# Performance work log

Hardware: AMD Instinct MI355X
Metric: run time of the kernel (lower is better)

## Reference

```python
import jax, jax.numpy as jnp
import numpy as np

B, T, J, D = 32, 1024, 256, 512

def setup_inputs() -> dict:
    key = jax.random.key(0)
    k1, k2, k3 = jax.random.split(key, 3)
    h = jax.random.normal(k1, (B, T, D), dtype=jnp.float32)
    u = jax.random.normal(k2, (B, J, D), dtype=jnp.float32)
    w = jax.random.normal(k3, (1, 3 * D), dtype=jnp.float32) * 0.05
    return {"h": h, "u": u, "w": w}

def reference(h, u, w):
    # S[b,i,j] = w . concat([h_i, u_j, h_i*u_j])
    # Algebraic decomposition: w = [w_h, w_u, w_m]
    d = h.shape[-1]
    w = w[0]
    w_h, w_u, w_m = w[:d], w[d:2*d], w[2*d:]
    # [B,T,1] + [B,1,J] + [B,T,J]
    term_h = jnp.einsum('btd,d->bt', h, w_h)[:, :, None]
    term_u = jnp.einsum('bjd,d->bj', u, w_u)[:, None, :]
    term_m = jnp.einsum('btd,bjd->btj', h * w_m, u)
    return term_h + term_u + term_m
```

## Files before the change

### kernel.cpp

```cpp
#include <hip/hip_runtime.h>
#include <hip/hip_bf16.h>
#include <stdint.h>

#define B_ 32
#define T_ 1024
#define J_ 256
#define D_ 512

typedef __attribute__((ext_vector_type(8))) short short8;
typedef __attribute__((ext_vector_type(4))) float floatx4;

__global__ __launch_bounds__(256) void prep_kernel(
    const float* __restrict__ h, const float* __restrict__ u,
    const float* __restrict__ w,
    __hip_bfloat16* __restrict__ A, __hip_bfloat16* __restrict__ Bu,
    float* __restrict__ th, float* __restrict__ tu)
{
    int row  = blockIdx.x * 4 + (threadIdx.x >> 6);
    int lane = threadIdx.x & 63;
    const float* src;
    const float* wsum;
    const float* wmul;
    __hip_bfloat16* dst;
    float* tdst;
    if (row < B_ * T_) {
        src  = h + (size_t)row * D_;
        wsum = w;
        wmul = w + 2 * D_;
        dst  = A + (size_t)row * D_;
        tdst = th + row;
    } else {
        int r = row - B_ * T_;
        src  = u + (size_t)r * D_;
        wsum = w + D_;
        wmul = nullptr;
        dst  = Bu + (size_t)r * D_;
        tdst = tu + r;
    }
    int base = lane * 8;
    float4 v0  = *(const float4*)(src  + base);
    float4 v1  = *(const float4*)(src  + base + 4);
    float4 ws0 = *(const float4*)(wsum + base);
    float4 ws1 = *(const float4*)(wsum + base + 4);
    float s = v0.x*ws0.x + v0.y*ws0.y + v0.z*ws0.z + v0.w*ws0.w
            + v1.x*ws1.x + v1.y*ws1.y + v1.z*ws1.z + v1.w*ws1.w;

    float vals[8] = {v0.x, v0.y, v0.z, v0.w, v1.x, v1.y, v1.z, v1.w};
    if (wmul) {
        float4 m0 = *(const float4*)(wmul + base);
        float4 m1 = *(const float4*)(wmul + base + 4);
        vals[0]*=m0.x; vals[1]*=m0.y; vals[2]*=m0.z; vals[3]*=m0.w;
        vals[4]*=m1.x; vals[5]*=m1.y; vals[6]*=m1.z; vals[7]*=m1.w;
    }
    union { __hip_bfloat16 b[8]; uint4 q; } pk;
#pragma unroll
    for (int i = 0; i < 8; i++) pk.b[i] = __float2bfloat16(vals[i]);
    *(uint4*)(dst + base) = pk.q;

#pragma unroll
    for (int off = 32; off > 0; off >>= 1) s += __shfl_down(s, off, 64);
    if (lane == 0) *tdst = s;
}

__device__ inline void gload_lds16(const void* g, void* l) {
    __builtin_amdgcn_global_load_lds(
        (__attribute__((address_space(1))) void*)(g),
        (__attribute__((address_space(3))) void*)(l),
        16, 0, 0);
}

__global__ __launch_bounds__(256) void gemm_kernel(
    const __hip_bfloat16* __restrict__ A,
    const __hip_bfloat16* __restrict__ Bu,
    const float* __restrict__ th,
    const float* __restrict__ tu,
    float* __restrict__ out)
{
    __shared__ __align__(16) __hip_bfloat16 sA[128 * 32];
    __shared__ __align__(16) __hip_bfloat16 sB[128 * 32];

    const int b   = blockIdx.y;
    const int tM  = blockIdx.x >> 1;
    const int tN  = blockIdx.x & 1;
    const int tid = threadIdx.x;
    const int w = tid >> 6, lane = tid & 63;
    const int wr = w >> 1, wc = w & 1;

    const __hip_bfloat16* Ab = A  + ((size_t)b * T_ + tM * 128) * D_;
    const __hip_bfloat16* Bb = Bu + ((size_t)b * J_ + tN * 128) * D_;

    const int sr = tid >> 2;
    const int sc = (tid & 3) * 8;
    const int ldsOff = tid * 8;

    floatx4 acc[4][4];
#pragma unroll
    for (int i = 0; i < 4; i++)
#pragma unroll
        for (int j = 0; j < 4; j++) acc[i][j] = (floatx4)0.0f;

    const int kb = (lane >> 4) * 8;
    const int fr = lane & 15;

    for (int k0 = 0; k0 < D_; k0 += 32) {
        gload_lds16(Ab + (size_t)sr        * D_ + k0 + sc, sA + ldsOff);
        gload_lds16(Ab + (size_t)(sr + 64) * D_ + k0 + sc, sA + 64 * 32 + ldsOff);
        gload_lds16(Bb + (size_t)sr        * D_ + k0 + sc, sB + ldsOff);
        gload_lds16(Bb + (size_t)(sr + 64) * D_ + k0 + sc, sB + 64 * 32 + ldsOff);
        __syncthreads();

        short8 af[4], bfr[4];
#pragma unroll
        for (int mi = 0; mi < 4; mi++)
            af[mi] = *(const short8*)(sA + (wr * 64 + mi * 16 + fr) * 32 + kb);
#pragma unroll
        for (int ni = 0; ni < 4; ni++)
            bfr[ni] = *(const short8*)(sB + (wc * 64 + ni * 16 + fr) * 32 + kb);
#pragma unroll
        for (int mi = 0; mi < 4; mi++)
#pragma unroll
            for (int ni = 0; ni < 4; ni++)
                acc[mi][ni] = __builtin_amdgcn_mfma_f32_16x16x32_bf16(
                    af[mi], bfr[ni], acc[mi][ni], 0, 0, 0);
        __syncthreads();
    }

    const size_t outB = (size_t)b * T_ * J_;
    const int colq = lane & 15;
    const int rq   = (lane >> 4) * 4;
    const float* thb = th + b * T_;
    const float* tub = tu + b * J_;
#pragma unroll
    for (int mi = 0; mi < 4; mi++) {
        int r0 = tM * 128 + wr * 64 + mi * 16 + rq;
#pragma unroll
        for (int ni = 0; ni < 4; ni++) {
            int col = tN * 128 + wc * 64 + ni * 16 + colq;
            float tuv = tub[col];
#pragma unroll
            for (int r = 0; r < 4; r++) {
                out[outB + (size_t)(r0 + r) * J_ + col] =
                    acc[mi][ni][r] + thb[r0 + r] + tuv;
            }
        }
    }
}

extern "C" void kernel_launch(void* const* d_in, const int* in_sizes, int n_in,
                              void* d_out, int out_size, void* d_ws, size_t ws_size,
                              hipStream_t stream)
{
    const float* h = (const float*)d_in[0];
    const float* u = (const float*)d_in[1];
    const float* w = (const float*)d_in[2];
    float* out = (float*)d_out;

    uint8_t* ws = (uint8_t*)d_ws;
    __hip_bfloat16* A  = (__hip_bfloat16*)ws;
    __hip_bfloat16* Bu = (__hip_bfloat16*)(ws + (size_t)B_*T_*D_*2);
    float* th = (float*)(ws + (size_t)B_*T_*D_*2 + (size_t)B_*J_*D_*2);
    float* tu = th + B_*T_;

    prep_kernel<<<dim3((B_*T_ + B_*J_) / 4), 256, 0, stream>>>(h, u, w, A, Bu, th, tu);

    gemm_kernel<<<dim3((T_/128)*(J_/128), B_), 256, 0, stream>>>(A, Bu, th, tu, out);
}
```

Baseline: 140.0 us.

## Fold w_h and w_m into u operand and read h directly in GEMM

Rewrites the score as h·(u*w_m + w_h) + u·w_u, so the h row term becomes part of the GEMM and only u needs preprocessing. The GEMM now loads fp32 h from global memory, converts it to bf16 in registers and stores it to LDS. This removes the large h-to-bf16 prep pass and its workspace round trip. The cost is that h tiles are reread in fp32 for each of the two N tiles, using synchronous loads without the async LDS path, and the h·w_h term now also goes through bf16 rounding.

```diff
diff --git a/kernel.cpp b/kernel.cpp
--- a/kernel.cpp
+++ b/kernel.cpp
@@ -10,56 +10,41 @@
 typedef __attribute__((ext_vector_type(8))) short short8;
 typedef __attribute__((ext_vector_type(4))) float floatx4;
 
-__global__ __launch_bounds__(256) void prep_kernel(
-    const float* __restrict__ h, const float* __restrict__ u,
-    const float* __restrict__ w,
-    __hip_bfloat16* __restrict__ A, __hip_bfloat16* __restrict__ Bu,
-    float* __restrict__ th, float* __restrict__ tu)
+__global__ __launch_bounds__(256) void prep_u_kernel(
+    const float* __restrict__ u, const float* __restrict__ w,
+    __hip_bfloat16* __restrict__ B2, float* __restrict__ tu)
 {
     int row  = blockIdx.x * 4 + (threadIdx.x >> 6);
     int lane = threadIdx.x & 63;
-    const float* src;
-    const float* wsum;
-    const float* wmul;
-    __hip_bfloat16* dst;
-    float* tdst;
-    if (row < B_ * T_) {
-        src  = h + (size_t)row * D_;
-        wsum = w;
-        wmul = w + 2 * D_;
-        dst  = A + (size_t)row * D_;
-        tdst = th + row;
-    } else {
-        int r = row - B_ * T_;
-        src  = u + (size_t)r * D_;
-        wsum = w + D_;
-        wmul = nullptr;
-        dst  = Bu + (size_t)r * D_;
-        tdst = tu + r;
-    }
+    const float* src = u + (size_t)row * D_;
     int base = lane * 8;
-    float4 v0  = *(const float4*)(src  + base);
-    float4 v1  = *(const float4*)(src  + base + 4);
-    float4 ws0 = *(const float4*)(wsum + base);
-    float4 ws1 = *(const float4*)(wsum + base + 4);
-    float s = v0.x*ws0.x + v0.y*ws0.y + v0.z*ws0.z + v0.w*ws0.w
-            + v1.x*ws1.x + v1.y*ws1.y + v1.z*ws1.z + v1.w*ws1.w;
 
-    float vals[8] = {v0.x, v0.y, v0.z, v0.w, v1.x, v1.y, v1.z, v1.w};
-    if (wmul) {
-        float4 m0 = *(const float4*)(wmul + base);
-        float4 m1 = *(const float4*)(wmul + base + 4);
-        vals[0]*=m0.x; vals[1]*=m0.y; vals[2]*=m0.z; vals[3]*=m0.w;
-        vals[4]*=m1.x; vals[5]*=m1.y; vals[6]*=m1.z; vals[7]*=m1.w;
-    }
+    float4 v0  = *(const float4*)(src + base);
+    float4 v1  = *(const float4*)(src + base + 4);
+    float4 wh0 = *(const float4*)(w + base);
+    float4 wh1 = *(const float4*)(w + base + 4);
+    float4 wu0 = *(const float4*)(w + D_ + base);
+    float4 wu1 = *(const float4*)(w + D_ + base + 4);
+    float4 wm0 = *(const float4*)(w + 2*D_ + base);
+    float4 wm1 = *(const float4*)(w + 2*D_ + base + 4);
+
+    float s = v0.x*wu0.x + v0.y*wu0.y + v0.z*wu0.z + v0.w*wu0.w
+            + v1.x*wu1.x + v1.y*wu1.y + v1.z*wu1.z + v1.w*wu1.w;
+
+    float vals[8] = {
+        v0.x*wm0.x + wh0.x, v0.y*wm0.y + wh0.y,
+        v0.z*wm0.z + wh0.z, v0.w*wm0.w + wh0.w,
+        v1.x*wm1.x + wh1.x, v1.y*wm1.y + wh1.y,
+        v1.z*wm1.z + wh1.z, v1.w*wm1.w + wh1.w };
+
     union { __hip_bfloat16 b[8]; uint4 q; } pk;
 #pragma unroll
     for (int i = 0; i < 8; i++) pk.b[i] = __float2bfloat16(vals[i]);
-    *(uint4*)(dst + base) = pk.q;
+    *(uint4*)(B2 + (size_t)row * D_ + base) = pk.q;
 
 #pragma unroll
     for (int off = 32; off > 0; off >>= 1) s += __shfl_down(s, off, 64);
-    if (lane == 0) *tdst = s;
+    if (lane == 0) tu[row] = s;
 }
 
 __device__ inline void gload_lds16(const void* g, void* l) {
@@ -70,9 +55,8 @@
 }
 
 __global__ __launch_bounds__(256) void gemm_kernel(
-    const __hip_bfloat16* __restrict__ A,
-    const __hip_bfloat16* __restrict__ Bu,
-    const float* __restrict__ th,
+    const float* __restrict__ h,
+    const __hip_bfloat16* __restrict__ B2,
     const float* __restrict__ tu,
     float* __restrict__ out)
 {
@@ -86,12 +70,15 @@
     const int w = tid >> 6, lane = tid & 63;
     const int wr = w >> 1, wc = w & 1;
 
-    const __hip_bfloat16* Ab = A  + ((size_t)b * T_ + tM * 128) * D_;
-    const __hip_bfloat16* Bb = Bu + ((size_t)b * J_ + tN * 128) * D_;
+    const float*          Ah = h  + ((size_t)b * T_ + tM * 128) * D_;
+    const __hip_bfloat16* Bb = B2 + ((size_t)b * J_ + tN * 128) * D_;
 
     const int sr = tid >> 2;
     const int sc = (tid & 3) * 8;
-    const int ldsOff = tid * 8;
+    const int ldsOffB = tid * 8;
+
+    const int ar = tid >> 1;
+    const int ac = (tid & 1) * 16;
 
     floatx4 acc[4][4];
 #pragma unroll
@@ -103,10 +90,28 @@
     const int fr = lane & 15;
 
     for (int k0 = 0; k0 < D_; k0 += 32) {
-        gload_lds16(Ab + (size_t)sr        * D_ + k0 + sc, sA + ldsOff);
-        gload_lds16(Ab + (size_t)(sr + 64) * D_ + k0 + sc, sA + 64 * 32 + ldsOff);
-        gload_lds16(Bb + (size_t)sr        * D_ + k0 + sc, sB + ldsOff);
-        gload_lds16(Bb + (size_t)(sr + 64) * D_ + k0 + sc, sB + 64 * 32 + ldsOff);
+        gload_lds16(Bb + (size_t)sr        * D_ + k0 + sc, sB + ldsOffB);
+        gload_lds16(Bb + (size_t)(sr + 64) * D_ + k0 + sc, sB + 64 * 32 + ldsOffB);
+
+        {
+            const float* ap = Ah + (size_t)ar * D_ + k0 + ac;
+            float4 a0 = *(const float4*)(ap);
+            float4 a1 = *(const float4*)(ap + 4);
+            float4 a2 = *(const float4*)(ap + 8);
+            float4 a3 = *(const float4*)(ap + 12);
+            union { __hip_bfloat16 b[16]; uint4 q[2]; } pk;
+            pk.b[0]=__float2bfloat16(a0.x); pk.b[1]=__float2bfloat16(a0.y);
+            pk.b[2]=__float2bfloat16(a0.z); pk.b[3]=__float2bfloat16(a0.w);
+            pk.b[4]=__float2bfloat16(a1.x); pk.b[5]=__float2bfloat16(a1.y);
+            pk.b[6]=__float2bfloat16(a1.z); pk.b[7]=__float2bfloat16(a1.w);
+            pk.b[8]=__float2bfloat16(a2.x); pk.b[9]=__float2bfloat16(a2.y);
+            pk.b[10]=__float2bfloat16(a2.z); pk.b[11]=__float2bfloat16(a2.w);
+            pk.b[12]=__float2bfloat16(a3.x); pk.b[13]=__float2bfloat16(a3.y);
+            pk.b[14]=__float2bfloat16(a3.z); pk.b[15]=__float2bfloat16(a3.w);
+            uint4* dst = (uint4*)(sA + ar * 32 + ac);
+            dst[0] = pk.q[0];
+            dst[1] = pk.q[1];
+        }
         __syncthreads();
 
         short8 af[4], bfr[4];
@@ -128,7 +133,6 @@
     const size_t outB = (size_t)b * T_ * J_;
     const int colq = lane & 15;
     const int rq   = (lane >> 4) * 4;
-    const float* thb = th + b * T_;
     const float* tub = tu + b * J_;
 #pragma unroll
     for (int mi = 0; mi < 4; mi++) {
@@ -140,7 +144,7 @@
 #pragma unroll
             for (int r = 0; r < 4; r++) {
                 out[outB + (size_t)(r0 + r) * J_ + col] =
-                    acc[mi][ni][r] + thb[r0 + r] + tuv;
+                    acc[mi][ni][r] + tuv;
             }
         }
     }
@@ -156,12 +160,10 @@
     float* out = (float*)d_out;
 
     uint8_t* ws = (uint8_t*)d_ws;
-    __hip_bfloat16* A  = (__hip_bfloat16*)ws;
-    __hip_bfloat16* Bu = (__hip_bfloat16*)(ws + (size_t)B_*T_*D_*2);
-    float* th = (float*)(ws + (size_t)B_*T_*D_*2 + (size_t)B_*J_*D_*2);
-    float* tu = th + B_*T_;
+    __hip_bfloat16* B2 = (__hip_bfloat16*)ws;
+    float* tu = (float*)(ws + (size_t)B_ * J_ * D_ * 2);
 
-    prep_kernel<<<dim3((B_*T_ + B_*J_) / 4), 256, 0, stream>>>(h, u, w, A, Bu, th, tu);
+    prep_u_kernel<<<dim3(B_ * J_ / 4), 256, 0, stream>>>(u, w, B2, tu);
 
-    gemm_kernel<<<dim3((T_/128)*(J_/128), B_), 256, 0, stream>>>(A, Bu, th, tu, out);
+    gemm_kernel<<<dim3((T_ / 128) * (J_ / 128), B_), 256, 0, stream>>>(h, B2, tu, out);
 }
```

Measured after the change: 136.6 us. 1.03x faster.
